# Kernel tuning notes

Measured on AMD Instinct MI355X. Metric: run time of the kernel, lower is better.

Reference implementation:

```python
import jax, jax.numpy as jnp
import numpy as np

B, S, D = 4, 2048, 1024  # batch, seq_len, input_dimension
KD, VD = 1024, 1024      # key_dim, value_dim


def setup_inputs() -> dict:
    key = jax.random.key(0)
    ks = jax.random.split(key, 9)
    sc_in = 1.0 / np.sqrt(D)
    sc_v = 1.0 / np.sqrt(VD)
    return {
        "x":  jax.random.normal(ks[0], (B, S, D), dtype=jnp.float32),
        "Wq": jax.random.normal(ks[1], (KD, D), dtype=jnp.float32) * sc_in,
        "bq": jax.random.normal(ks[2], (KD,), dtype=jnp.float32) * 0.01,
        "Wk": jax.random.normal(ks[3], (KD, D), dtype=jnp.float32) * sc_in,
        "bk": jax.random.normal(ks[4], (KD,), dtype=jnp.float32) * 0.01,
        "Wv": jax.random.normal(ks[5], (VD, D), dtype=jnp.float32) * sc_in,
        "bv": jax.random.normal(ks[6], (VD,), dtype=jnp.float32) * 0.01,
        "Wo": jax.random.normal(ks[7], (D, VD), dtype=jnp.float32) * sc_v,
        "bo": jax.random.normal(ks[8], (D,), dtype=jnp.float32) * 0.01,
    }


def reference(x, Wq, bq, Wk, bk, Wv, bv, Wo, bo):
    # projections (torch Linear: x @ W.T + b)
    q = jnp.einsum('bsd,kd->bsk', x, Wq) + bq   # (B,S,KD)
    k = jnp.einsum('bsd,kd->bsk', x, Wk) + bk   # (B,S,KD)
    v = jnp.einsum('bsd,vd->bsv', x, Wv) + bv   # (B,S,VD)

    scores = jnp.einsum('bqk,bsk->bqs', q, k) / jnp.sqrt(jnp.float32(KD))  # (B,S,S)

    # sign rescale: scores * sign(scores) (sign(0) mapped to 1) == |scores| with zeros kept
    sign_mask = jnp.sign(scores)
    sign_mask = sign_mask + (sign_mask == 0).astype(jnp.float32)

    # causal mask: lower-triangular (incl diag) multiplied by 1, strict upper -> -inf
    seq = scores.shape[-1]
    causal = jnp.tril(jnp.ones((seq, seq), dtype=bool))
    masked = jnp.where(causal, scores * sign_mask, -jnp.inf)

    weights = jax.nn.softmax(masked, axis=2)            # (B,S,S)
    out = jnp.einsum('bqs,bsv->bqv', weights, v)        # (B,S,VD)
    return jnp.einsum('bqv,dv->bqd', out, Wo) + bo      # (B,S,D)
```

## Files before the change

kernel.cpp:

```cpp
#include <hip/hip_runtime.h>
#include <hip/hip_bf16.h>
#include <cstdint>


typedef __attribute__((ext_vector_type(8))) __bf16 bf16x8;
typedef __attribute__((ext_vector_type(4))) __bf16 bf16x4;
typedef __attribute__((ext_vector_type(4))) float floatx4;

struct Ptr3 { const float* p[3]; };

__device__ __forceinline__ void async_copy16(const __bf16* g, const __bf16* l) {
  __builtin_amdgcn_global_load_lds(
      (const __attribute__((address_space(1))) unsigned int*)(const void*)g,
      (__attribute__((address_space(3))) unsigned int*)(unsigned)(uintptr_t)(const void*)l,
      16, 0, 0);
}

__device__ __forceinline__ void gemm_core8p(const __bf16* __restrict__ pA,
                                            const __bf16* __restrict__ pB,
                                            int K, int nT, int mb, int nb,
                                            floatx4 (&acc)[8][4]) {
  __shared__ __align__(16) __bf16 As[2][16384];
  __shared__ __align__(16) __bf16 Bs[2][16384];

  const int t = threadIdx.x;
  const int lane = t & 63;
  const int wave = t >> 6;
  const int quad = lane >> 4;
  const int l16 = lane & 15;
  const int wm = wave >> 2;
  const int wn = wave & 3;

  const int r0 = t >> 3;
  const int csw = ((t & 7) ^ (r0 & 7)) * 8;
  const __bf16* gA = pA + (long)(mb * 256 + r0) * K + csw;
  const __bf16* gB = pB + (long)(nb * 256 + r0) * K + csw;
  const long row64 = (long)64 * K;
  const long row128 = (long)128 * K;

  auto stageA = [&](int kt, int half) {
    const long ko = (long)kt * 64 + (long)half * row128;
    __bf16* d = &As[kt & 1][half * 8192 + t * 8];
    async_copy16(gA + ko, d);
    async_copy16(gA + ko + row64, d + 4096);
  };
  auto stageB = [&](int kt, int half) {
    const long ko = (long)kt * 64 + (long)half * row128;
    __bf16* d = &Bs[kt & 1][half * 8192 + t * 8];
    async_copy16(gB + ko, d);
    async_copy16(gB + ko + row64, d + 4096);
  };
  auto cl = [&](int kt) { return kt < nT ? kt : nT - 1; };

  bf16x8 af[4][2], bfr[2][2];
  auto ldsA = [&](int buf, int ihalf) {
#pragma unroll
    for (int i2 = 0; i2 < 4; ++i2) {
      const int rl = wm * 64 + i2 * 16 + l16;
      const int rb = ihalf * 8192 + rl * 64;
      const int key = rl & 7;
#pragma unroll
      for (int ks = 0; ks < 2; ++ks)
        af[i2][ks] = *(const bf16x8*)&As[buf][rb + (((ks * 4 + quad) ^ key) << 3)];
    }
  };
  auto ldsB = [&](int buf, int jhalf) {
#pragma unroll
    for (int j2 = 0; j2 < 2; ++j2) {
      const int rl = wn * 32 + j2 * 16 + l16;
      const int rb = jhalf * 8192 + rl * 64;
      const int key = rl & 7;
#pragma unroll
      for (int ks = 0; ks < 2; ++ks)
        bfr[j2][ks] = *(const bf16x8*)&Bs[buf][rb + (((ks * 4 + quad) ^ key) << 3)];
    }
  };
  auto mfmaQ = [&](int ihalf, int jhalf) {
    __builtin_amdgcn_s_setprio(1);
#pragma unroll
    for (int ks = 0; ks < 2; ++ks)
#pragma unroll
      for (int i2 = 0; i2 < 4; ++i2)
#pragma unroll
        for (int j2 = 0; j2 < 2; ++j2)
          acc[ihalf * 4 + i2][jhalf * 2 + j2] =
              __builtin_amdgcn_mfma_f32_16x16x32_bf16(
                  af[i2][ks], bfr[j2][ks],
                  acc[ihalf * 4 + i2][jhalf * 2 + j2], 0, 0, 0);
    __builtin_amdgcn_s_setprio(0);
  };

#define VM6 asm volatile("s_waitcnt vmcnt(6)" ::: "memory")
#define PHASE(LDSOP, STAGEOP, WAITOP, IH, JH)                 \
  LDSOP;                                                      \
  STAGEOP;                                                    \
  WAITOP;                                                     \
  __builtin_amdgcn_sched_barrier(0);                          \
  __builtin_amdgcn_s_barrier();                               \
  asm volatile("s_waitcnt lgkmcnt(0)" ::: "memory");          \
  __builtin_amdgcn_sched_barrier(0);                          \
  mfmaQ(IH, JH);                                              \
  __builtin_amdgcn_s_barrier();

  stageA(0, 0); stageB(0, 0); stageB(0, 1); stageA(0, 1);
  stageA(1, 0); stageB(1, 1); stageA(1, 1);
  VM6;
  __builtin_amdgcn_s_barrier();
  __builtin_amdgcn_sched_barrier(0);

  const int nIter = nT >> 1;
  for (int it = 0, T = 0; it < nIter; ++it, T += 2) {
    PHASE((ldsA(0, 0), ldsB(0, 0)), stageB(cl(T + 1), 0), (void)0, 0, 0)
    PHASE(ldsB(0, 1),               stageA(cl(T + 2), 0), (void)0, 0, 1)
    PHASE(ldsA(0, 1),               stageB(cl(T + 2), 1), (void)0, 1, 1)
    PHASE(ldsB(0, 0),               stageA(cl(T + 2), 1), VM6,     1, 0)
    PHASE((ldsA(1, 0), ldsB(1, 0)), stageB(cl(T + 2), 0), (void)0, 0, 0)
    PHASE(ldsB(1, 1),               stageA(cl(T + 3), 0), (void)0, 0, 1)
    PHASE(ldsA(1, 1),               stageB(cl(T + 3), 1), (void)0, 1, 1)
    PHASE(ldsB(1, 0),               stageA(cl(T + 3), 1), VM6,     1, 0)
  }
  __syncthreads();
#undef PHASE
#undef VM6
}


__global__ void prepW(const float* __restrict__ Wo, Ptr3 tp,
                      const float* __restrict__ bv, const float* __restrict__ bq,
                      const float* __restrict__ bk,
                      __bf16* __restrict__ Wob, __bf16* __restrict__ Wqt,
                      __bf16* __restrict__ Wkt, __bf16* __restrict__ Wvt,
                      float* __restrict__ bvo, float* __restrict__ cscal,
                      float* __restrict__ lsum) {
  __shared__ __bf16 tile[64][66];
  __shared__ float wsum[4];
  const int bid = blockIdx.x;
  const int t = threadIdx.x;
  if (bid < 1024) {
    const long e = ((long)bid * 256 + t) * 4;
    const float4 f = *(const float4*)(Wo + e);
    bf16x4 o;
    o[0] = (__bf16)f.x; o[1] = (__bf16)f.y; o[2] = (__bf16)f.z; o[3] = (__bf16)f.w;
    *(bf16x4*)(Wob + e) = o;
  } else if (bid < 1792) {
    const int seg = (bid - 1024) >> 8;
    const int idx = (bid - 1024) & 255;
    const float* src = tp.p[seg];
    __bf16* dstw = seg == 0 ? Wqt : (seg == 1 ? Wkt : Wvt);
    const int r0 = (idx >> 4) * 64, c0 = (idx & 15) * 64;
#pragma unroll
    for (int e = 0; e < 16; ++e) {
      const int i = e * 256 + t;
      const int r = i >> 6, c = i & 63;
      tile[r][c] = (__bf16)src[(long)(r0 + r) * 1024 + (c0 + c)];
    }
    __syncthreads();
#pragma unroll
    for (int e = 0; e < 16; ++e) {
      const int i = e * 256 + t;
      const int r = i >> 6, c = i & 63;
      dstw[(long)(c0 + r) * 1024 + (r0 + c)] = tile[c][r];
    }
  } else if (bid < 2816) {
    const int d = bid - 1792;
    const float* row = Wo + (long)d * 1024;
    float s = 0.f;
    for (int v = t; v < 1024; v += 256) s += bv[v] * row[v];
#pragma unroll
    for (int off = 32; off > 0; off >>= 1) s += __shfl_down(s, off, 64);
    if ((t & 63) == 0) wsum[t >> 6] = s;
    __syncthreads();
    if (t == 0) bvo[d] = wsum[0] + wsum[1] + wsum[2] + wsum[3];
  } else if (bid == 2816) {
    float s = 0.f;
    for (int i = t; i < 1024; i += 256) s += bq[i] * bk[i];
#pragma unroll
    for (int off = 32; off > 0; off >>= 1) s += __shfl_down(s, off, 64);
    if ((t & 63) == 0) wsum[t >> 6] = s;
    __syncthreads();
    if (t == 0) *cscal = wsum[0] + wsum[1] + wsum[2] + wsum[3];
  } else {
#pragma unroll
    for (int e = 0; e < 8; ++e)
      *(float4*)(lsum + (e * 256 + t) * 4) = float4{0.f, 0.f, 0.f, 0.f};
  }
}

__global__ void __launch_bounds__(512, 2)
gemmWX(const __bf16* __restrict__ Wkt, const __bf16* __restrict__ Wqt,
       const __bf16* __restrict__ Wob, const __bf16* __restrict__ Wvt,
       __bf16* __restrict__ Mt, __bf16* __restrict__ Wvo,
       const float* __restrict__ bk, const float* __restrict__ bq,
       float* __restrict__ m1f, float* __restrict__ m2f,
       const float* __restrict__ x, __bf16* __restrict__ xb) {
  const int id = blockIdx.x;
  const int t = threadIdx.x;

  if (id >= 64) {
    const long i = ((long)(id - 64) * 512 + t) * 4;
    const float4 f = *(const float4*)(x + i);
    bf16x4 o;
    o[0] = (__bf16)f.x; o[1] = (__bf16)f.y; o[2] = (__bf16)f.z; o[3] = (__bf16)f.w;
    *(bf16x4*)(xb + i) = o;
    return;
  }
  if (id >= 32) {
    const int g = id - 32;
    const bool isM2 = g >= 16;
    const int q = g & 15;
    const __bf16* Wt = isM2 ? Wkt : Wqt;
    const float* bvec = isM2 ? bq : bk;
    float* dst = isM2 ? m2f : m1f;
    const int row = q * 64 + (t >> 3);
    const int l8 = t & 7;
    const __bf16* wr = Wt + (long)row * 1024 + l8 * 128;
    const float* bp = bvec + l8 * 128;
    float s = 0.f;
#pragma unroll
    for (int jj = 0; jj < 16; ++jj) {
      bf16x8 wv = *(const bf16x8*)(wr + jj * 8);
#pragma unroll
      for (int e = 0; e < 8; ++e) s += (float)wv[e] * bp[jj * 8 + e];
    }
    s += __shfl_xor(s, 1, 64);
    s += __shfl_xor(s, 2, 64);
    s += __shfl_xor(s, 4, 64);
    if (l8 == 0) dst[row] = s;
    return;
  }

  const bool isMt = id < 16;
  const int w = isMt ? id : id - 16;
  const int mb = w >> 2, nb = w & 3;
  const __bf16* pA = isMt ? Wkt : Wob;
  const __bf16* pB = isMt ? Wqt : Wvt;
  __bf16* dst = isMt ? Mt : Wvo;

  floatx4 acc[8][4] = {};
  gemm_core8p(pA, pB, 1024, 16, mb, nb, acc);

  const int lane = t & 63, wave = t >> 6;
  const int quad = lane >> 4, l16 = lane & 15;
  const int wm = wave >> 2, wn = wave & 3;
#pragma unroll
  for (int j = 0; j < 4; ++j) {
    const int gc = nb * 256 + (j >> 1) * 128 + wn * 32 + (j & 1) * 16 + l16;
#pragma unroll
    for (int i = 0; i < 8; ++i) {
      const int gr = mb * 256 + (i >> 2) * 128 + wm * 64 + (i & 3) * 16 + quad * 4;
#pragma unroll
      for (int r = 0; r < 4; ++r)
        dst[(long)(gr + r) * 1024 + gc] = (__bf16)acc[i][j][r];
    }
  }
}

__global__ void __launch_bounds__(512, 2)
big1(const __bf16* __restrict__ xb, const __bf16* __restrict__ Mt,
     const __bf16* __restrict__ Wvo, const float* __restrict__ m2f,
     const float* __restrict__ bvo, __bf16* __restrict__ y2,
     __bf16* __restrict__ Ut, const float* __restrict__ m1f,
     const float* __restrict__ cscal, float* __restrict__ uvec,
     int S, int D) {
  const int id = blockIdx.x;
  const int t = threadIdx.x;

  if (id >= 256) {
    const int k = id - 256;
    const int row = k * 64 + (t >> 3);
    const int l8 = t & 7;
    const float c = *cscal;
    const __bf16* xr = xb + (long)row * 1024 + l8 * 128;
    const float* mp = m1f + l8 * 128;
    float s = 0.f;
#pragma unroll
    for (int jj = 0; jj < 16; ++jj) {
      bf16x8 xv = *(const bf16x8*)(xr + jj * 8);
#pragma unroll
      for (int e = 0; e < 8; ++e) s += (float)xv[e] * mp[jj * 8 + e];
    }
    s += __shfl_xor(s, 1, 64);
    s += __shfl_xor(s, 2, 64);
    s += __shfl_xor(s, 4, 64);
    if (l8 == 0) uvec[row] = s + c;
    return;
  }

  const bool isY2 = id < 128;
  const int w = isY2 ? id : id - 128;
  const int mb = w >> 2;
  const int nb = w & 3;
  const __bf16* pB = isY2 ? Mt : Wvo;

  floatx4 acc[8][4] = {};
  gemm_core8p(xb, pB, 1024, 16, mb, nb, acc);

  const int lane = t & 63, wave = t >> 6;
  const int quad = lane >> 4, l16 = lane & 15;
  const int wm = wave >> 2, wn = wave & 3;

  if (isY2) {
#pragma unroll
    for (int j = 0; j < 4; ++j) {
      const int gc = nb * 256 + (j >> 1) * 128 + wn * 32 + (j & 1) * 16 + l16;
      const float bvv = m2f[gc];
#pragma unroll
      for (int i = 0; i < 8; ++i) {
        const int gr = mb * 256 + (i >> 2) * 128 + wm * 64 + (i & 3) * 16 + quad * 4;
#pragma unroll
        for (int r = 0; r < 4; ++r)
          y2[(long)(gr + r) * 1024 + gc] = (__bf16)(acc[i][j][r] + bvv);
      }
    }
  } else {
    const int bb = (mb * 256) / S;
    const int s0 = mb * 256 - bb * S;
#pragma unroll
    for (int j = 0; j < 4; ++j) {
      const int gc = nb * 256 + (j >> 1) * 128 + wn * 32 + (j & 1) * 16 + l16;
      const float bv = bvo[gc];
#pragma unroll
      for (int i = 0; i < 8; ++i) {
        const int sr = s0 + (i >> 2) * 128 + wm * 64 + (i & 3) * 16 + quad * 4;
        bf16x4 o;
#pragma unroll
        for (int r = 0; r < 4; ++r) o[r] = (__bf16)(acc[i][j][r] + bv);
        *(bf16x4*)&Ut[((long)bb * D + gc) * S + sr] = o;
      }
    }
  }
}

__global__ void __launch_bounds__(512, 2)
scoresP(const __bf16* __restrict__ xb, const __bf16* __restrict__ y2,
        const float* __restrict__ uvec, __bf16* __restrict__ P,
        float* __restrict__ lsum, int S, int KD) {
  const int id = blockIdx.x;
  const int b = id / 36;
  const int r = id - b * 36;
  int mb = 0;
  while ((mb + 1) * (mb + 2) / 2 <= r) ++mb;
  const int nb = r - mb * (mb + 1) / 2;

  floatx4 acc[8][4] = {};
  gemm_core8p(y2 + (long)b * S * KD, xb + (long)b * S * KD, KD, 16, mb, nb, acc);

  const int t = threadIdx.x;
  const int lane = t & 63, wave = t >> 6;
  const int quad = lane >> 4, l16 = lane & 15;
  const int wm = wave >> 2, wn = wave & 3;

  __bf16* C = P + (long)b * S * S;
  float* lrow = lsum + (long)b * S;
  const float sc = 0.03125f;
#pragma unroll
  for (int i = 0; i < 8; ++i) {
#pragma unroll
    for (int r4 = 0; r4 < 4; ++r4) {
      const int row = mb * 256 + (i >> 2) * 128 + wm * 64 + (i & 3) * 16 + quad * 4 + r4;
      const float urow = uvec[(long)b * S + row];
      float psum = 0.f;
#pragma unroll
      for (int j = 0; j < 4; ++j) {
        const int col = nb * 256 + (j >> 1) * 128 + wn * 32 + (j & 1) * 16 + l16;
        const float p =
            (col <= row) ? __expf(fabsf(acc[i][j][r4] + urow) * sc) : 0.f;
        psum += p;
        C[(long)row * S + col] = (__bf16)p;
      }
      psum += __shfl_xor(psum, 1, 64);
      psum += __shfl_xor(psum, 2, 64);
      psum += __shfl_xor(psum, 4, 64);
      psum += __shfl_xor(psum, 8, 64);
      if (l16 == 0) atomicAdd(&lrow[row], psum);
    }
  }
}

__global__ void __launch_bounds__(512, 2)
pvoS(const __bf16* __restrict__ P, const __bf16* __restrict__ Ut,
     const float* __restrict__ lsum, const float* __restrict__ bo,
     float* __restrict__ out, float* __restrict__ part, int S, int D) {
  const int id = blockIdx.x;
  const int t = threadIdx.x;

  const __bf16 *pA, *pB;
  int nT, mb, nb, b, khalf = 0;
  bool heavy;
  if (id < 128) {
    heavy = true;
    khalf = id & 1;
    const int rest = id >> 1;
    nb = rest & 3;
    const int mbh = (rest >> 2) & 3;
    b = rest >> 4;
    mb = 4 + mbh;
    nT = 2 * (mb + 1);
    const long koff = (long)khalf * nT * 64;
    pA = P + (long)b * S * S + koff;
    pB = Ut + (long)b * D * S + koff;
  } else {
    heavy = false;
    const int l = id - 128;
    nb = l & 3;
    mb = (l >> 2) & 3;
    b = l >> 4;
    nT = 4 * (mb + 1);
    pA = P + (long)b * S * S;
    pB = Ut + (long)b * D * S;
  }

  floatx4 acc[8][4] = {};
  gemm_core8p(pA, pB, S, nT, mb, nb, acc);

  const int lane = t & 63, wave = t >> 6;
  const int quad = lane >> 4, l16 = lane & 15;
  const int wm = wave >> 2, wn = wave & 3;

  if (heavy) {
    float* ps = part + ((long)((b * 4 + (mb - 4)) * 2 + khalf)) * 256 * 1024;
#pragma unroll
    for (int i = 0; i < 8; ++i) {
#pragma unroll
      for (int r = 0; r < 4; ++r) {
        const int lr = (i >> 2) * 128 + wm * 64 + (i & 3) * 16 + quad * 4 + r;
#pragma unroll
        for (int j = 0; j < 4; ++j) {
          const int col = nb * 256 + (j >> 1) * 128 + wn * 32 + (j & 1) * 16 + l16;
          ps[(long)lr * 1024 + col] = acc[i][j][r];
        }
      }
    }
  } else {
    const float* lrow = lsum + (long)b * S;
#pragma unroll
    for (int i = 0; i < 8; ++i) {
#pragma unroll
      for (int r = 0; r < 4; ++r) {
        const int row = mb * 256 + (i >> 2) * 128 + wm * 64 + (i & 3) * 16 + quad * 4 + r;
        const float inv = 1.f / lrow[row];
#pragma unroll
        for (int j = 0; j < 4; ++j) {
          const int col = nb * 256 + (j >> 1) * 128 + wn * 32 + (j & 1) * 16 + l16;
          out[((long)b * S + row) * D + col] = acc[i][j][r] * inv + bo[col];
        }
      }
    }
  }
}

__global__ void combineH(const float* __restrict__ part,
                         const float* __restrict__ lsum,
                         const float* __restrict__ bo, float* __restrict__ out,
                         int S, int D) {
  const int hr = blockIdx.x;
  const int t = threadIdx.x;
  const int b = hr >> 10;
  const int lr = hr & 1023;
  const int mbh = lr >> 8;
  const int r256 = lr & 255;
  const int srow = (4 + mbh) * 256 + r256;
  const float inv = 1.f / lsum[(long)b * S + srow];
  const long base = (long)((b * 4 + mbh) * 2) * 256 * 1024 + (long)r256 * 1024;
  const float4 p0 = *(const float4*)(part + base + t * 4);
  const float4 p1 = *(const float4*)(part + base + 256 * 1024 + t * 4);
  const float4 bv = *(const float4*)(bo + t * 4);
  float4 o;
  o.x = (p0.x + p1.x) * inv + bv.x;
  o.y = (p0.y + p1.y) * inv + bv.y;
  o.z = (p0.z + p1.z) * inv + bv.z;
  o.w = (p0.w + p1.w) * inv + bv.w;
  *(float4*)(out + ((long)b * S + srow) * D + t * 4) = o;
}

extern "C" void kernel_launch(void* const* d_in, const int* in_sizes, int n_in,
                              void* d_out, int out_size, void* d_ws, size_t ws_size,
                              hipStream_t stream) {
  const float* x = (const float*)d_in[0];
  const float* Wq = (const float*)d_in[1];
  const float* bq = (const float*)d_in[2];
  const float* Wk = (const float*)d_in[3];
  const float* bk = (const float*)d_in[4];
  const float* Wv = (const float*)d_in[5];
  const float* bv = (const float*)d_in[6];
  const float* Wo = (const float*)d_in[7];
  const float* bo = (const float*)d_in[8];
  float* out = (float*)d_out;

  constexpr int B = 4, S = 2048, D = 1024, KD = 1024;
  constexpr long MB_ = 1024 * 1024;

  char* w = (char*)d_ws;
  __bf16* xb  = (__bf16*)(w);
  __bf16* y2  = (__bf16*)(w + 16 * MB_);
  __bf16* Ut  = (__bf16*)(w + 32 * MB_);
  __bf16* P   = (__bf16*)(w + 48 * MB_);
  __bf16* Wob = (__bf16*)(w + 80 * MB_);
  __bf16* Wqt = (__bf16*)(w + 82 * MB_);
  __bf16* Wkt = (__bf16*)(w + 84 * MB_);
  __bf16* Wvt = (__bf16*)(w + 86 * MB_);
  __bf16* Mt  = (__bf16*)(w + 88 * MB_);
  __bf16* Wvo = (__bf16*)(w + 90 * MB_);
  float* lsum  = (float*)(w + 92 * MB_);
  float* uvec  = (float*)(w + 92 * MB_ + 32768);
  float* bvo   = (float*)(w + 92 * MB_ + 65536);
  float* m2f   = (float*)(w + 92 * MB_ + 69632);
  float* m1f   = (float*)(w + 92 * MB_ + 73728);
  float* cscal = (float*)(w + 92 * MB_ + 77824);
  float* part  = (float*)(w);

  Ptr3 tp{{Wq, Wk, Wv}};
  prepW<<<2818, 256, 0, stream>>>(Wo, tp, bv, bq, bk, Wob, Wqt, Wkt, Wvt,
                                  bvo, cscal, lsum);

  gemmWX<<<4160, 512, 0, stream>>>(Wkt, Wqt, Wob, Wvt, Mt, Wvo, bk, bq,
                                   m1f, m2f, x, xb);

  big1<<<384, 512, 0, stream>>>(xb, Mt, Wvo, m2f, bvo, y2, Ut, m1f, cscal,
                                uvec, S, D);

  scoresP<<<144, 512, 0, stream>>>(xb, y2, uvec, P, lsum, S, KD);

  pvoS<<<192, 512, 0, stream>>>(P, Ut, lsum, bo, out, part, S, D);

  combineH<<<4096, 256, 0, stream>>>(part, lsum, bo, out, S, D);
}
```

Baseline: 253.3 us.

## Split-K the weight-product GEMMs across more blocks and add a reduction kernel

Measured after the change: 255.3 us. No clear change (+0.8%).

```diff
diff --git a/kernel.cpp b/kernel.cpp
--- a/kernel.cpp
+++ b/kernel.cpp
@@ -91,22 +91,20 @@
   };
 
 #define VM6 asm volatile("s_waitcnt vmcnt(6)" ::: "memory")
+#define LGKM0 asm volatile("s_waitcnt lgkmcnt(0)" ::: "memory")
 #define PHASE(LDSOP, STAGEOP, WAITOP, IH, JH)                 \
   LDSOP;                                                      \
   STAGEOP;                                                    \
   WAITOP;                                                     \
-  __builtin_amdgcn_sched_barrier(0);                          \
   __builtin_amdgcn_s_barrier();                               \
-  asm volatile("s_waitcnt lgkmcnt(0)" ::: "memory");          \
-  __builtin_amdgcn_sched_barrier(0);                          \
   mfmaQ(IH, JH);                                              \
+  LGKM0;                                                      \
   __builtin_amdgcn_s_barrier();
 
   stageA(0, 0); stageB(0, 0); stageB(0, 1); stageA(0, 1);
   stageA(1, 0); stageB(1, 1); stageA(1, 1);
   VM6;
   __builtin_amdgcn_s_barrier();
-  __builtin_amdgcn_sched_barrier(0);
 
   const int nIter = nT >> 1;
   for (int it = 0, T = 0; it < nIter; ++it, T += 2) {
@@ -122,6 +120,7 @@
   __syncthreads();
 #undef PHASE
 #undef VM6
+#undef LGKM0
 }
 
 
@@ -189,23 +188,23 @@
 __global__ void __launch_bounds__(512, 2)
 gemmWX(const __bf16* __restrict__ Wkt, const __bf16* __restrict__ Wqt,
        const __bf16* __restrict__ Wob, const __bf16* __restrict__ Wvt,
-       __bf16* __restrict__ Mt, __bf16* __restrict__ Wvo,
+       float* __restrict__ partW,
        const float* __restrict__ bk, const float* __restrict__ bq,
        float* __restrict__ m1f, float* __restrict__ m2f,
        const float* __restrict__ x, __bf16* __restrict__ xb) {
   const int id = blockIdx.x;
   const int t = threadIdx.x;
 
-  if (id >= 64) {
-    const long i = ((long)(id - 64) * 512 + t) * 4;
+  if (id >= 160) {
+    const long i = ((long)(id - 160) * 512 + t) * 4;
     const float4 f = *(const float4*)(x + i);
     bf16x4 o;
     o[0] = (__bf16)f.x; o[1] = (__bf16)f.y; o[2] = (__bf16)f.z; o[3] = (__bf16)f.w;
     *(bf16x4*)(xb + i) = o;
     return;
   }
-  if (id >= 32) {
-    const int g = id - 32;
+  if (id >= 128) {
+    const int g = id - 128;
     const bool isM2 = g >= 16;
     const int q = g & 15;
     const __bf16* Wt = isM2 ? Wkt : Wqt;
@@ -229,16 +228,18 @@
     return;
   }
 
-  const bool isMt = id < 16;
-  const int w = isMt ? id : id - 16;
-  const int mb = w >> 2, nb = w & 3;
-  const __bf16* pA = isMt ? Wkt : Wob;
-  const __bf16* pB = isMt ? Wqt : Wvt;
-  __bf16* dst = isMt ? Mt : Wvo;
+  const int mat = id >> 6;
+  const int w = id & 63;
+  const int kc = w & 3;
+  const int nb = (w >> 2) & 3;
+  const int mb = w >> 4;
+  const __bf16* pA = (mat ? Wob : Wkt) + kc * 256;
+  const __bf16* pB = (mat ? Wvt : Wqt) + kc * 256;
 
   floatx4 acc[8][4] = {};
-  gemm_core8p(pA, pB, 1024, 16, mb, nb, acc);
-
+  gemm_core8p(pA, pB, 1024, 4, mb, nb, acc);
+
+  float* ps = partW + ((long)(mat * 4 + kc) << 20);
   const int lane = t & 63, wave = t >> 6;
   const int quad = lane >> 4, l16 = lane & 15;
   const int wm = wave >> 2, wn = wave & 3;
@@ -250,9 +251,26 @@
       const int gr = mb * 256 + (i >> 2) * 128 + wm * 64 + (i & 3) * 16 + quad * 4;
 #pragma unroll
       for (int r = 0; r < 4; ++r)
-        dst[(long)(gr + r) * 1024 + gc] = (__bf16)acc[i][j][r];
-    }
-  }
+        ps[(long)(gr + r) * 1024 + gc] = acc[i][j][r];
+    }
+  }
+}
+
+__global__ void combW(const float* __restrict__ partW, __bf16* __restrict__ Mt,
+                      __bf16* __restrict__ Wvo) {
+  const long idx4 = (long)blockIdx.x * 256 + threadIdx.x;
+  const int mat = idx4 >= 262144;
+  const long local = (idx4 - (long)mat * 262144) * 4;
+  const float* base = partW + ((long)mat * 4 << 20);
+  float4 s = *(const float4*)(base + local);
+#pragma unroll
+  for (int kc = 1; kc < 4; ++kc) {
+    const float4 p = *(const float4*)(base + ((long)kc << 20) + local);
+    s.x += p.x; s.y += p.y; s.z += p.z; s.w += p.w;
+  }
+  bf16x4 o;
+  o[0] = (__bf16)s.x; o[1] = (__bf16)s.y; o[2] = (__bf16)s.z; o[3] = (__bf16)s.w;
+  *(bf16x4*)((mat ? Wvo : Mt) + local) = o;
 }
 
 __global__ void __launch_bounds__(512, 2)
@@ -508,13 +526,16 @@
   float* m1f   = (float*)(w + 92 * MB_ + 73728);
   float* cscal = (float*)(w + 92 * MB_ + 77824);
   float* part  = (float*)(w);
+  float* partW = (float*)(w + 48 * MB_);
 
   Ptr3 tp{{Wq, Wk, Wv}};
   prepW<<<2818, 256, 0, stream>>>(Wo, tp, bv, bq, bk, Wob, Wqt, Wkt, Wvt,
                                   bvo, cscal, lsum);
 
-  gemmWX<<<4160, 512, 0, stream>>>(Wkt, Wqt, Wob, Wvt, Mt, Wvo, bk, bq,
+  gemmWX<<<4256, 512, 0, stream>>>(Wkt, Wqt, Wob, Wvt, partW, bk, bq,
                                    m1f, m2f, x, xb);
+
+  combW<<<2048, 256, 0, stream>>>(partW, Mt, Wvo);
 
   big1<<<384, 512, 0, stream>>>(xb, Mt, Wvo, m2f, bvo, y2, Ut, m1f, cscal,
                                 uvec, S, D);
```
